# Kernel tuning notes

Measured on AMD Instinct MI355X. Metric: run time of the kernel, lower is better.

## Reference

```python
import math
import jax, jax.numpy as jnp
import numpy as np

D_MODEL = 256
NUM_FEATURES = 512  # 2 * d_model (module default)
BATCH, SEQ = 4, 4096
EPS = 1e-6
INPUT_SCALE = 0.25  # keeps exp(xW/sqrt(d) - ||x||^2/2) numerically meaningful


def _make_projection(key):
    # Orthogonal random features: ceil(M/d)=2 QR blocks, then sqrt(|gauss|) row scaling.
    k1, k2, k3 = jax.random.split(key, 3)
    q1, _ = jnp.linalg.qr(jax.random.normal(k1, (D_MODEL, D_MODEL), jnp.float32))
    q2, _ = jnp.linalg.qr(jax.random.normal(k2, (D_MODEL, D_MODEL), jnp.float32))
    proj = jnp.concatenate([q1, q2], axis=1)[:, :NUM_FEATURES]  # (d, M)
    scaling = jnp.sqrt(jnp.abs(jax.random.normal(k3, (D_MODEL, 1), jnp.float32)))
    return proj * scaling


def setup_inputs() -> dict:
    key = jax.random.key(0)
    kq, kk, kv, kp = jax.random.split(key, 4)
    shape = (BATCH, SEQ, D_MODEL)
    return {
        "query": jax.random.normal(kq, shape, jnp.float32) * INPUT_SCALE,
        "key": jax.random.normal(kk, shape, jnp.float32) * INPUT_SCALE,
        "value": jax.random.normal(kv, shape, jnp.float32) * INPUT_SCALE,
        "projection": _make_projection(kp),  # (d_model, num_features) buffer
    }


def _phi(x, projection):
    # phi(x) = exp(xW/sqrt(d) - ||x||^2/2) / sqrt(M)
    d = x.shape[-1]
    m = projection.shape[-1]
    proj = jnp.matmul(x, projection) / math.sqrt(d)  # (B, L, M)
    sq = 0.5 * jnp.sum(x * x, axis=-1, keepdims=True)  # (B, L, 1)
    return jnp.exp(proj - sq) / math.sqrt(m)


def reference(query, key, value, projection):
    qp = _phi(query, projection)  # (B, L, M)
    kp = _phi(key, projection)    # (B, L, M)
    B, L, M = qp.shape
    D = value.shape[-1]

    # Causal linear attention: running KV-state scan, O(B*M*D) state
    # (same math as cumsum of k' (outer) v, without materializing (B,L,M,D)).
    def step(carry, inp):
        kv_state, k_state = carry  # (B,M,D), (B,M)
        q_t, k_t, v_t = inp        # (B,M), (B,M), (B,D)
        kv_state = kv_state + k_t[:, :, None] * v_t[:, None, :]
        k_state = k_state + k_t
        num = jnp.einsum('bm,bmd->bd', q_t, kv_state)
        den = jnp.einsum('bm,bm->b', q_t, k_state)[:, None] + EPS
        return (kv_state, k_state), num / den

    init = (jnp.zeros((B, M, D), qp.dtype), jnp.zeros((B, M), qp.dtype))
    xs = (jnp.swapaxes(qp, 0, 1), jnp.swapaxes(kp, 0, 1), jnp.swapaxes(value, 0, 1))
    _, out = jax.lax.scan(step, init, xs)  # (L, B, D)
    return jnp.swapaxes(out, 0, 1)  # (B, L, D)
```

## Files before the change

kernel.cpp:

```cpp
#include <hip/hip_runtime.h>

#define B_ 4
#define L_ 4096
#define D_ 256
#define M_ 512
#define C_ 256
#define NC_ 16
#define NG_ (B_*NC_)
#define EPS_ 1e-6f
#define RSQRT_D_ 0.0625f
#define RSQRT_M_ 0.044194173824159216f

typedef __attribute__((ext_vector_type(8))) short short8;
typedef __attribute__((ext_vector_type(4))) short short4v;
typedef __attribute__((ext_vector_type(4))) float floatx4;

__device__ __forceinline__ short f2b(float f) {
  union { float f; unsigned u; } c; c.f = f;
  unsigned r = c.u + 0x7fffu + ((c.u >> 16) & 1u);
  return (short)(r >> 16);
}
__device__ __forceinline__ float b2f(short s) {
  union { unsigned u; float f; } c; c.u = ((unsigned)(unsigned short)s) << 16;
  return c.f;
}

__device__ __forceinline__ void async_copy16(const short* g, short* l) {
  __builtin_amdgcn_global_load_lds(
      (const __attribute__((address_space(1))) void*)(g),
      (__attribute__((address_space(3))) void*)(l), 16, 0, 0);
}

#define OFF_SB   0u
#define OFF_WT   16777216u
#define OFF_QP   17039360u
#define OFF_KP   33816576u
#define OFF_KPT  50593792u
#define OFF_VT   67371008u
#define OFF_AM   75759616u
#define OFF_PB   84148224u
#define OFF_ZP   100925440u

__device__ __forceinline__ void mfma_tile_gemm(
    const short* __restrict__ Ag, int lda,
    const short* __restrict__ Bg, int ldb,
    int K, short* sA, short* sB, floatx4 acc[4][4])
{
  const int tid  = threadIdx.x;
  const int lane = tid & 63;
  const int wave = tid >> 6;
  const int wm = wave >> 1, wn = wave & 1;
  const int q = lane >> 4, ml = lane & 15;

  for (int k0 = 0; k0 < K; k0 += 64) {
    #pragma unroll
    for (int it = 0; it < 4; ++it) {
      int s = tid + 256 * it;
      int m = s >> 3, k8 = s & 7;
      async_copy16(Ag + (size_t)m * lda + k0 + k8 * 8, sA + s * 8);
      async_copy16(Bg + (size_t)m * ldb + k0 + k8 * 8, sB + s * 8);
    }
    __syncthreads();
    #pragma unroll
    for (int ks = 0; ks < 2; ++ks) {
      short8 a[4], b[4];
      int k8 = ks * 4 + q;
      #pragma unroll
      for (int i = 0; i < 4; ++i) {
        int ra = wm * 64 + i * 16 + ml;
        a[i] = *(const short8*)(sA + (ra * 8 + k8) * 8);
        int rb = wn * 64 + i * 16 + ml;
        b[i] = *(const short8*)(sB + (rb * 8 + k8) * 8);
      }
      #pragma unroll
      for (int i = 0; i < 4; ++i)
        #pragma unroll
        for (int j = 0; j < 4; ++j)
          acc[i][j] = __builtin_amdgcn_mfma_f32_16x16x32_bf16(a[i], b[j], acc[i][j], 0, 0, 0);
    }
    __syncthreads();
  }
}

__global__ __launch_bounds__(256) void transpose_cvt_kernel(
    const float* __restrict__ v, const float* __restrict__ W,
    short* __restrict__ vT, short* __restrict__ Wt)
{
  const int z = blockIdx.z;
  const float* src; short* dst; int ld_in, ld_out;
  if (z < NG_) {
    if (blockIdx.x >= 4) return;
    src = v + (size_t)z * (C_*D_) + (size_t)blockIdx.y * 64 * D_ + blockIdx.x * 64;
    dst = vT + (size_t)z * (D_*C_) + (size_t)blockIdx.x * 64 * C_ + blockIdx.y * 64;
    ld_in = D_; ld_out = C_;
  } else {
    src = W + (size_t)blockIdx.y * 64 * M_ + blockIdx.x * 64;
    dst = Wt + (size_t)blockIdx.x * 64 * D_ + blockIdx.y * 64;
    ld_in = M_; ld_out = D_;
  }
  __shared__ short sm[64 * 65];
  const int tid = threadIdx.x;
  #pragma unroll
  for (int it = 0; it < 4; ++it) {
    int ci = tid + 256 * it;
    int row = ci >> 4, c4 = ci & 15;
    float4 x = *(const float4*)(src + (size_t)row * ld_in + c4 * 4);
    sm[(c4 * 4 + 0) * 65 + row] = f2b(x.x);
    sm[(c4 * 4 + 1) * 65 + row] = f2b(x.y);
    sm[(c4 * 4 + 2) * 65 + row] = f2b(x.z);
    sm[(c4 * 4 + 3) * 65 + row] = f2b(x.w);
  }
  __syncthreads();
  #pragma unroll
  for (int it = 0; it < 2; ++it) {
    int ci = tid + 256 * it;
    int dr = ci >> 3, t8 = ci & 7;
    short8 o;
    #pragma unroll
    for (int u = 0; u < 8; ++u) o[u] = sm[dr * 65 + t8 * 8 + u];
    *(short8*)(dst + (size_t)dr * ld_out + t8 * 8) = o;
  }
}

__global__ __launch_bounds__(512) void phi_mfma_kernel(
    const float* __restrict__ qin, const float* __restrict__ kin,
    const short* __restrict__ Wt,
    short* __restrict__ qp, short* __restrict__ kp, short* __restrict__ kpT,
    float* __restrict__ ZP)
{
  const bool is_k = (blockIdx.z == 1);
  const float* X = is_k ? kin : qin;
  short* outP = is_k ? kp : qp;
  const int idl = blockIdx.x + 2 * blockIdx.y;
  const int row0 = ((idl & 7) + 8 * (idl >> 4)) * 128;
  const int col0 = ((idl >> 3) & 1) * 256;
  __shared__ short smem[34816];
  __shared__ float zsb[512];
  __shared__ float sqs[128];
  short* sA = smem;
  short* sB = smem + 8192;
  const int tid = threadIdx.x, lane = tid & 63, wave = tid >> 6;
  const int wm = wave >> 2, wn = wave & 3, q = lane >> 4, ml = lane & 15;
  const int c8 = tid & 7, r8 = tid >> 3;
  floatx4 acc[4][4];
  #pragma unroll
  for (int i = 0; i < 4; ++i)
    #pragma unroll
    for (int j = 0; j < 4; ++j) acc[i][j] = (floatx4){0.f,0.f,0.f,0.f};

  float4 px0[2], px1[2];
  #pragma unroll
  for (int it = 0; it < 2; ++it) {
    const float* src = X + (size_t)(row0 + r8 + 64 * it) * D_ + c8 * 8;
    px0[it] = *(const float4*)src;
    px1[it] = *(const float4*)(src + 4);
  }
  short8 pw[4];
  #pragma unroll
  for (int it = 0; it < 4; ++it) {
    int mm = r8 + 64 * it;
    pw[it] = *(const short8*)(Wt + (size_t)(col0 + mm) * D_ + c8 * 8);
  }
  float ssq[2] = {0.f, 0.f};
  for (int k0 = 0; k0 < D_; k0 += 64) {
    #pragma unroll
    for (int it = 0; it < 2; ++it) {
      int m = r8 + 64 * it;
      float4 x0 = px0[it], x1 = px1[it];
      short8 vv;
      vv[0] = f2b(x0.x); vv[1] = f2b(x0.y); vv[2] = f2b(x0.z); vv[3] = f2b(x0.w);
      vv[4] = f2b(x1.x); vv[5] = f2b(x1.y); vv[6] = f2b(x1.z); vv[7] = f2b(x1.w);
      ssq[it] += x0.x*x0.x + x0.y*x0.y + x0.z*x0.z + x0.w*x0.w
               + x1.x*x1.x + x1.y*x1.y + x1.z*x1.z + x1.w*x1.w;
      *(short8*)(sA + (c8 * 128 + (m ^ c8)) * 8) = vv;
    }
    #pragma unroll
    for (int it = 0; it < 4; ++it) {
      int mm = r8 + 64 * it;
      *(short8*)(sB + (c8 * 256 + (mm ^ c8)) * 8) = pw[it];
    }
    if (k0 + 64 < D_) {
      #pragma unroll
      for (int it = 0; it < 2; ++it) {
        const float* src = X + (size_t)(row0 + r8 + 64 * it) * D_ + k0 + 64 + c8 * 8;
        px0[it] = *(const float4*)src;
        px1[it] = *(const float4*)(src + 4);
      }
      #pragma unroll
      for (int it = 0; it < 4; ++it) {
        int mm = r8 + 64 * it;
        pw[it] = *(const short8*)(Wt + (size_t)(col0 + mm) * D_ + k0 + 64 + c8 * 8);
      }
    }
    __syncthreads();
    #pragma unroll
    for (int ks = 0; ks < 2; ++ks) {
      short8 a[4], b[4];
      int kk = ks * 4 + q;
      #pragma unroll
      for (int i = 0; i < 4; ++i) {
        int ra = (wm * 64 + i * 16 + ml) ^ kk;
        a[i] = *(const short8*)(sA + (kk * 128 + ra) * 8);
        int rb = (wn * 64 + i * 16 + ml) ^ kk;
        b[i] = *(const short8*)(sB + (kk * 256 + rb) * 8);
      }
      #pragma unroll
      for (int i = 0; i < 4; ++i)
        #pragma unroll
        for (int j = 0; j < 4; ++j)
          acc[i][j] = __builtin_amdgcn_mfma_f32_16x16x32_bf16(a[i], b[j], acc[i][j], 0, 0, 0);
    }
    __syncthreads();
  }
  #pragma unroll
  for (int o = 1; o < 8; o <<= 1)
    #pragma unroll
    for (int it = 0; it < 2; ++it) ssq[it] += __shfl_xor(ssq[it], o);
  if (c8 == 0) {
    sqs[r8] = 0.5f * ssq[0];
    sqs[r8 + 64] = 0.5f * ssq[1];
  }
  __syncthreads();

  if (!is_k) {
    #pragma unroll
    for (int i = 0; i < 4; ++i) {
      int rl = wm * 64 + i * 16 + q * 4;
      float sqv[4];
      #pragma unroll
      for (int r = 0; r < 4; ++r) sqv[r] = sqs[rl + r];
      #pragma unroll
      for (int j = 0; j < 4; ++j) {
        int cl = wn * 64 + j * 16 + ml;
        #pragma unroll
        for (int r = 0; r < 4; ++r) {
          float pv = __expf(fmaf(acc[i][j][r], RSQRT_D_, -sqv[r])) * RSQRT_M_;
          smem[(size_t)(rl + r) * 264 + cl] = f2b(pv);
        }
      }
    }
    __syncthreads();
    #pragma unroll
    for (int it = 0; it < 8; ++it) {
      int idx = tid + 512 * it;
      int row = idx >> 5, cc8 = idx & 31;
      short8 vv = *(const short8*)(smem + (size_t)row * 264 + cc8 * 8);
      *(short8*)(outP + (size_t)(row0 + row) * M_ + col0 + cc8 * 8) = vv;
    }
  } else {
    float csum[4] = {0.f, 0.f, 0.f, 0.f};
    #pragma unroll
    for (int i = 0; i < 4; ++i) {
      int rl = wm * 64 + i * 16 + q * 4;
      float sqv[4];
      #pragma unroll
      for (int r = 0; r < 4; ++r) sqv[r] = sqs[rl + r];
      #pragma unroll
      for (int j = 0; j < 4; ++j) {
        int cl = wn * 64 + j * 16 + ml;
        short4v tb;
        #pragma unroll
        for (int r = 0; r < 4; ++r) {
          float pv = __expf(fmaf(acc[i][j][r], RSQRT_D_, -sqv[r])) * RSQRT_M_;
          short bv = f2b(pv);
          outP[(size_t)(row0 + rl + r) * M_ + col0 + cl] = bv;
          tb[r] = bv;
          csum[j] += b2f(bv);
        }
        *(short4v*)(smem + (size_t)cl * 136 + rl) = tb;
      }
    }
    #pragma unroll
    for (int j = 0; j < 4; ++j) {
      csum[j] += __shfl_xor(csum[j], 16);
      csum[j] += __shfl_xor(csum[j], 32);
    }
    if (lane < 16) {
      #pragma unroll
      for (int j = 0; j < 4; ++j)
        zsb[wm * 256 + wn * 64 + j * 16 + ml] = csum[j];
    }
    __syncthreads();
    int g = row0 >> 8, tb0 = row0 & 255;
    #pragma unroll
    for (int it = 0; it < 8; ++it) {
      int ci = tid + 512 * it;
      int t8 = ci & 15, cc = ci >> 4;
      short8 vv = *(const short8*)(smem + (size_t)cc * 136 + t8 * 8);
      *(short8*)(kpT + (size_t)g * (M_*C_) + (size_t)(col0 + cc) * C_ + tb0 + t8 * 8) = vv;
    }
    if (tid < 256) {
      float s = zsb[tid] + zsb[256 + tid];
      int p = (row0 >> 7) & 1;
      ZP[((size_t)g * 2 + p) * M_ + col0 + tid] = s;
    }
  }
}

__global__ __launch_bounds__(256) void mega_kernel(
    const short* __restrict__ vT, const short* __restrict__ kpT,
    const short* __restrict__ qp, const short* __restrict__ kp,
    short* __restrict__ Sb, short* __restrict__ Am)
{
  const int id = blockIdx.x + 4 * blockIdx.y + 12 * blockIdx.z;
  const int t12 = id >> 3;
  const int g  = (id & 7) + 8 * (t12 / 12);
  const int inner = t12 % 12;
  const int bx = inner & 3, by = inner >> 2;
  __shared__ short smem[17408];
  const int tid = threadIdx.x;

  floatx4 acc[4][4];
  #pragma unroll
  for (int i = 0; i < 4; ++i)
    #pragma unroll
    for (int j = 0; j < 4; ++j) acc[i][j] = (floatx4){0.f,0.f,0.f,0.f};
  const int lane = tid & 63, wave = tid >> 6;
  const int wm = wave >> 1, wn = wave & 1, q = lane >> 4, ln = lane & 15;

  if (by < 2) {
    const int m0 = bx * 128, d0 = by * 128;
    mfma_tile_gemm(vT + (size_t)g * (D_*C_) + (size_t)d0 * C_, C_,
                   kpT + (size_t)g * (M_*C_) + (size_t)m0 * C_, C_, C_,
                   smem, smem + 8192, acc);
    #pragma unroll
    for (int i = 0; i < 4; ++i) {
      int lr = wm * 64 + i * 16 + q * 4;
      #pragma unroll
      for (int j = 0; j < 4; ++j) {
        int lc = wn * 64 + j * 16 + ln;
        #pragma unroll
        for (int r = 0; r < 4; ++r)
          smem[(size_t)(lr + r) * 136 + lc] = f2b(acc[i][j][r]);
      }
    }
    __syncthreads();
    #pragma unroll
    for (int it = 0; it < 8; ++it) {
      int idx = tid + 256 * it;
      int row = idx >> 4, c8 = idx & 15;
      short8 vv = *(const short8*)(smem + (size_t)row * 136 + c8 * 8);
      *(short8*)(Sb + ((size_t)g * D_ + d0 + row) * M_ + m0 + c8 * 8) = vv;
    }
  } else {
    const int tt0 = (bx >> 1) * 128, tp0 = (bx & 1) * 128;
    short* Ag = Am + (size_t)g * (C_*C_);
    if (tp0 > tt0) {
      short8 z8 = 0;
      #pragma unroll
      for (int it = 0; it < 8; ++it) {
        int ci = tid + 256 * it;
        int row = ci >> 4, c8 = ci & 15;
        *(short8*)(Ag + (size_t)(tt0 + row) * C_ + tp0 + c8 * 8) = z8;
      }
      return;
    }
    const size_t cb = (size_t)g * C_;
    mfma_tile_gemm(qp + (cb + tt0) * M_, M_, kp + (cb + tp0) * M_, M_, M_,
                   smem, smem + 8192, acc);
    #pragma unroll
    for (int i = 0; i < 4; ++i) {
      int lr = wm * 64 + i * 16 + q * 4;
      #pragma unroll
      for (int j = 0; j < 4; ++j) {
        int lc = wn * 64 + j * 16 + ln;
        #pragma unroll
        for (int r = 0; r < 4; ++r) {
          short bv = ((tp0 + lc) <= (tt0 + lr + r)) ? f2b(acc[i][j][r]) : (short)0;
          smem[(size_t)(lr + r) * 136 + lc] = bv;
        }
      }
    }
    __syncthreads();
    #pragma unroll
    for (int it = 0; it < 8; ++it) {
      int idx = tid + 256 * it;
      int row = idx >> 4, c8 = idx & 15;
      short8 vv = *(const short8*)(smem + (size_t)row * 136 + c8 * 8);
      *(short8*)(Ag + (size_t)(tt0 + row) * C_ + tp0 + c8 * 8) = vv;
    }
  }
}

__global__ __launch_bounds__(256) void prefixS_kernel(
    const short* __restrict__ Sb, short* __restrict__ Pb,
    const float* __restrict__ ZP, float* __restrict__ ZPX)
{
  if (blockIdx.x >= 256) {
    int idx = (blockIdx.x - 256) * 256 + threadIdx.x;
    int b = idx >> 9, m = idx & 511;
    float run = 0.f;
    #pragma unroll
    for (int i = 0; i < NC_; ++i) {
      int g = b * NC_ + i;
      ZPX[(size_t)g * M_ + m] = run;
      run += ZP[((size_t)g * 2 + 0) * M_ + m] + ZP[((size_t)g * 2 + 1) * M_ + m];
    }
    return;
  }
  int j = blockIdx.x * 256 + threadIdx.x;
  int b = j >> 14, e8 = j & 16383;
  size_t base = ((size_t)b * NC_) * 131072 + (size_t)e8 * 8;
  short8 t[NC_];
  #pragma unroll
  for (int i = 0; i < NC_; ++i)
    t[i] = *(const short8*)(Sb + base + (size_t)i * 131072);
  float run[8] = {0.f,0.f,0.f,0.f,0.f,0.f,0.f,0.f};
  #pragma unroll
  for (int i = 0; i < NC_; ++i) {
    short8 o;
    #pragma unroll
    for (int u = 0; u < 8; ++u) { o[u] = f2b(run[u]); run[u] += b2f(t[i][u]); }
    *(short8*)(Pb + base + (size_t)i * 131072) = o;
  }
}

__global__ __launch_bounds__(256) void out_mfma_kernel(
    const short* __restrict__ qp, const short* __restrict__ Pb,
    const short* __restrict__ Am, const short* __restrict__ vT,
    const float* __restrict__ ZPX, float* __restrict__ out)
{
  const int id = blockIdx.x + 2 * blockIdx.y + 8 * blockIdx.z;
  const int g  = (id & 7) + 8 * (id >> 6);
  const int inner = (id >> 3) & 7;
  const int d0 = (inner & 1) * 128, tt0 = (inner >> 1) * 64;
  __shared__ short smem[16896];
  __shared__ float zbuf[512];
  __shared__ float dbuf[64];
  short* sA = smem; short* sB = smem + 4096;
  const int tid = threadIdx.x, lane = tid & 63, wave = tid >> 6;
  const int wm = wave >> 1, wn = wave & 1, q = lane >> 4, ml = lane & 15;
  const int r8 = tid >> 3;

  {
    zbuf[tid]       = ZPX[(size_t)g * M_ + tid];
    zbuf[tid + 256] = ZPX[(size_t)g * M_ + 256 + tid];
    if (tid < 64) dbuf[tid] = 0.f;
  }
  __syncthreads();

  floatx4 acc[2][4];
  #pragma unroll
  for (int i = 0; i < 2; ++i)
    #pragma unroll
    for (int j = 0; j < 4; ++j) acc[i][j] = (floatx4){0.f,0.f,0.f,0.f};

  {
    const short* Ag = qp + ((size_t)g * C_ + tt0) * M_;
    const short* Bg = Pb + (size_t)g * (D_*M_) + (size_t)d0 * M_;
    float dp[2] = {0.f, 0.f};
    short8 pa[2], pb[4];
    #pragma unroll
    for (int it = 0; it < 2; ++it) {
      int ci = tid + 256 * it;
      int m = ci >> 3, k8 = ci & 7;
      pa[it] = *(const short8*)(Ag + (size_t)m * M_ + k8 * 8);
    }
    #pragma unroll
    for (int it = 0; it < 4; ++it) {
      int ci = tid + 256 * it;
      int m = ci >> 3, k8 = ci & 7;
      pb[it] = *(const short8*)(Bg + (size_t)m * M_ + k8 * 8);
    }
    for (int k0 = 0; k0 < M_; k0 += 64) {
      #pragma unroll
      for (int it = 0; it < 2; ++it) {
        int ci = tid + 256 * it;
        int m = ci >> 3, k8 = ci & 7;
        int dst = (k8 >> 2) * 256 + (m >> 4) * 64 + (k8 & 3) * 16 + ((m & 15) ^ k8);
        *(short8*)(sA + dst * 8) = pa[it];
        const float* zz = zbuf + k0 + k8 * 8;
        float d = 0.f;
        #pragma unroll
        for (int u = 0; u < 8; ++u) d = fmaf(b2f(pa[it][u]), zz[u], d);
        dp[it] += d;
      }
      #pragma unroll
      for (int it = 0; it < 4; ++it) {
        int ci = tid + 256 * it;
        int m = ci >> 3, k8 = ci & 7;
        int dst = (k8 >> 2) * 512 + (m >> 4) * 64 + (k8 & 3) * 16 + ((m & 15) ^ k8);
        *(short8*)(sB + dst * 8) = pb[it];
      }
      if (k0 + 64 < M_) {
        #pragma unroll
        for (int it = 0; it < 2; ++it) {
          int ci = tid + 256 * it;
          int m = ci >> 3, k8 = ci & 7;
          pa[it] = *(const short8*)(Ag + (size_t)m * M_ + k0 + 64 + k8 * 8);
        }
        #pragma unroll
        for (int it = 0; it < 4; ++it) {
          int ci = tid + 256 * it;
          int m = ci >> 3, k8 = ci & 7;
          pb[it] = *(const short8*)(Bg + (size_t)m * M_ + k0 + 64 + k8 * 8);
        }
      }
      __syncthreads();
      #pragma unroll
      for (int ks = 0; ks < 2; ++ks) {
        short8 a[2], b[4];
        int k8 = ks * 4 + q;
        #pragma unroll
        for (int i = 0; i < 2; ++i) {
          int ca = ks * 256 + (wm * 2 + i) * 64 + q * 16 + (ml ^ k8);
          a[i] = *(const short8*)(sA + ca * 8);
        }
        #pragma unroll
        for (int j = 0; j < 4; ++j) {
          int cb = ks * 512 + (wn * 4 + j) * 64 + q * 16 + (ml ^ k8);
          b[j] = *(const short8*)(sB + cb * 8);
        }
        #pragma unroll
        for (int i = 0; i < 2; ++i)
          #pragma unroll
          for (int j = 0; j < 4; ++j)
            acc[i][j] = __builtin_amdgcn_mfma_f32_16x16x32_bf16(a[i], b[j], acc[i][j], 0, 0, 0);
      }
      __syncthreads();
    }
    #pragma unroll
    for (int o = 1; o < 8; o <<= 1)
      #pragma unroll
      for (int it = 0; it < 2; ++it) dp[it] += __shfl_xor(dp[it], o);
    if ((tid & 7) == 0) {
      #pragma unroll
      for (int it = 0; it < 2; ++it) dbuf[r8 + 32 * it] += dp[it];
    }
  }

  {
    const short* Ag = Am + ((size_t)g * C_ + tt0) * C_;
    const short* Bg = vT + (size_t)g * (D_*C_) + (size_t)d0 * C_;
    float dp[2] = {0.f, 0.f};
    short8 pa[2], pb[4];
    #pragma unroll
    for (int it = 0; it < 2; ++it) {
      int ci = tid + 256 * it;
      int m = ci >> 3, k8 = ci & 7;
      pa[it] = *(const short8*)(Ag + (size_t)m * C_ + k8 * 8);
    }
    #pragma unroll
    for (int it = 0; it < 4; ++it) {
      int ci = tid + 256 * it;
      int m = ci >> 3, k8 = ci & 7;
      pb[it] = *(const short8*)(Bg + (size_t)m * C_ + k8 * 8);
    }
    for (int k0 = 0; k0 < C_; k0 += 64) {
      #pragma unroll
      for (int it = 0; it < 2; ++it) {
        int ci = tid + 256 * it;
        int m = ci >> 3, k8 = ci & 7;
        int dst = (k8 >> 2) * 256 + (m >> 4) * 64 + (k8 & 3) * 16 + ((m & 15) ^ k8);
        *(short8*)(sA + dst * 8) = pa[it];
        float d = 0.f;
        #pragma unroll
        for (int u = 0; u < 8; ++u) d += b2f(pa[it][u]);
        dp[it] += d;
      }
      #pragma unroll
      for (int it = 0; it < 4; ++it) {
        int ci = tid + 256 * it;
        int m = ci >> 3, k8 = ci & 7;
        int dst = (k8 >> 2) * 512 + (m >> 4) * 64 + (k8 & 3) * 16 + ((m & 15) ^ k8);
        *(short8*)(sB + dst * 8) = pb[it];
      }
      if (k0 + 64 < C_) {
        #pragma unroll
        for (int it = 0; it < 2; ++it) {
          int ci = tid + 256 * it;
          int m = ci >> 3, k8 = ci & 7;
          pa[it] = *(const short8*)(Ag + (size_t)m * C_ + k0 + 64 + k8 * 8);
        }
        #pragma unroll
        for (int it = 0; it < 4; ++it) {
          int ci = tid + 256 * it;
          int m = ci >> 3, k8 = ci & 7;
          pb[it] = *(const short8*)(Bg + (size_t)m * C_ + k0 + 64 + k8 * 8);
        }
      }
      __syncthreads();
      #pragma unroll
      for (int ks = 0; ks < 2; ++ks) {
        short8 a[2], b[4];
        int k8 = ks * 4 + q;
        #pragma unroll
        for (int i = 0; i < 2; ++i) {
          int ca = ks * 256 + (wm * 2 + i) * 64 + q * 16 + (ml ^ k8);
          a[i] = *(const short8*)(sA + ca * 8);
        }
        #pragma unroll
        for (int j = 0; j < 4; ++j) {
          int cb = ks * 512 + (wn * 4 + j) * 64 + q * 16 + (ml ^ k8);
          b[j] = *(const short8*)(sB + cb * 8);
        }
        #pragma unroll
        for (int i = 0; i < 2; ++i)
          #pragma unroll
          for (int j = 0; j < 4; ++j)
            acc[i][j] = __builtin_amdgcn_mfma_f32_16x16x32_bf16(a[i], b[j], acc[i][j], 0, 0, 0);
      }
      __syncthreads();
    }
    #pragma unroll
    for (int o = 1; o < 8; o <<= 1)
      #pragma unroll
      for (int it = 0; it < 2; ++it) dp[it] += __shfl_xor(dp[it], o);
    if ((tid & 7) == 0) {
      #pragma unroll
      for (int it = 0; it < 2; ++it) dbuf[r8 + 32 * it] += dp[it];
    }
  }
  __syncthreads();

  float* smF = (float*)smem;
  #pragma unroll
  for (int i = 0; i < 2; ++i) {
    int lr = wm * 32 + i * 16 + q * 4;
    #pragma unroll
    for (int r = 0; r < 4; ++r) {
      float rc = 1.0f / (dbuf[lr + r] + EPS_);
      #pragma unroll
      for (int j = 0; j < 4; ++j) {
        int lc = wn * 64 + j * 16 + ml;
        smF[(size_t)(lr + r) * 132 + lc] = acc[i][j][r] * rc;
      }
    }
  }
  __syncthreads();
  #pragma unroll
  for (int it = 0; it < 8; ++it) {
    int idx = tid + 256 * it;
    int row = idx >> 5, c4 = idx & 31;
    float4 val = *(const float4*)(smF + (size_t)row * 132 + c4 * 4);
    *(float4*)(out + (size_t)(g * C_ + tt0 + row) * D_ + d0 + c4 * 4) = val;
  }
}

extern "C" void kernel_launch(void* const* d_in, const int* in_sizes, int n_in,
                              void* d_out, int out_size, void* d_ws, size_t ws_size,
                              hipStream_t stream) {
  const float* q = (const float*)d_in[0];
  const float* k = (const float*)d_in[1];
  const float* v = (const float*)d_in[2];
  const float* W = (const float*)d_in[3];
  float* out = (float*)d_out;
  char* ws = (char*)d_ws;

  short* Sb  = (short*)(ws + OFF_SB);
  short* Wt  = (short*)(ws + OFF_WT);
  short* qp  = (short*)(ws + OFF_QP);
  short* kp  = (short*)(ws + OFF_KP);
  short* kpT = (short*)(ws + OFF_KPT);
  short* vT  = (short*)(ws + OFF_VT);
  short* Am  = (short*)(ws + OFF_AM);
  short* Pb  = (short*)(ws + OFF_PB);
  float* ZP  = (float*)(ws + OFF_ZP);
  float* ZPX = (float*)(ws + OFF_WT);

  transpose_cvt_kernel<<<dim3(8, 4, NG_ + 1), 256, 0, stream>>>(v, W, vT, Wt);
  phi_mfma_kernel<<<dim3(2, 128, 2), 512, 0, stream>>>(q, k, Wt, qp, kp, kpT, ZP);
  mega_kernel<<<dim3(4, 3, NG_), 256, 0, stream>>>(vT, kpT, qp, kp, Sb, Am);
  prefixS_kernel<<<264, 256, 0, stream>>>(Sb, Pb, ZP, ZPX);
  out_mfma_kernel<<<dim3(2, 4, NG_), 256, 0, stream>>>(qp, Pb, Am, vT, ZPX, out);
}
```

Baseline: 159.3 us.

## Register-prefetch GEMM tiles with swizzled LDS and lighter barriers

The shared mfma_tile_gemm drops the global_load_lds async copies. It now prefetches the next K-tile into registers while the current tile sits in LDS, and stores it with an XOR-swizzled layout to cut LDS bank conflicts. Across all GEMM loops, __syncthreads is replaced by a custom barrier that waits only on lgkmcnt (LDS) before s_barrier, so outstanding global prefetch loads are not drained at each barrier. This raises register pressure, and correctness now depends on the compiler inserting vmcnt waits before the prefetched registers are used.

Result: no change. 157.3 us (-1.2%).

```diff
diff --git a/kernel.cpp b/kernel.cpp
--- a/kernel.cpp
+++ b/kernel.cpp
@@ -25,10 +25,8 @@
   return c.f;
 }
 
-__device__ __forceinline__ void async_copy16(const short* g, short* l) {
-  __builtin_amdgcn_global_load_lds(
-      (const __attribute__((address_space(1))) void*)(g),
-      (__attribute__((address_space(3))) void*)(l), 16, 0, 0);
+__device__ __forceinline__ void wg_barrier_lgkm() {
+  asm volatile("s_waitcnt lgkmcnt(0)\n\ts_barrier" ::: "memory");
 }
 
 #define OFF_SB   0u
@@ -52,25 +50,43 @@
   const int wm = wave >> 1, wn = wave & 1;
   const int q = lane >> 4, ml = lane & 15;
 
+  short8 pa[4], pb[4];
+  #pragma unroll
+  for (int it = 0; it < 4; ++it) {
+    int ci = tid + 256 * it;
+    int m = ci >> 3, k8 = ci & 7;
+    pa[it] = *(const short8*)(Ag + (size_t)m * lda + k8 * 8);
+    pb[it] = *(const short8*)(Bg + (size_t)m * ldb + k8 * 8);
+  }
   for (int k0 = 0; k0 < K; k0 += 64) {
     #pragma unroll
     for (int it = 0; it < 4; ++it) {
-      int s = tid + 256 * it;
-      int m = s >> 3, k8 = s & 7;
-      async_copy16(Ag + (size_t)m * lda + k0 + k8 * 8, sA + s * 8);
-      async_copy16(Bg + (size_t)m * ldb + k0 + k8 * 8, sB + s * 8);
-    }
-    __syncthreads();
+      int ci = tid + 256 * it;
+      int m = ci >> 3, k8 = ci & 7;
+      int dst = (k8 >> 2) * 512 + (m >> 4) * 64 + (k8 & 3) * 16 + ((m & 15) ^ k8);
+      *(short8*)(sA + dst * 8) = pa[it];
+      *(short8*)(sB + dst * 8) = pb[it];
+    }
+    if (k0 + 64 < K) {
+      #pragma unroll
+      for (int it = 0; it < 4; ++it) {
+        int ci = tid + 256 * it;
+        int m = ci >> 3, k8 = ci & 7;
+        pa[it] = *(const short8*)(Ag + (size_t)m * lda + k0 + 64 + k8 * 8);
+        pb[it] = *(const short8*)(Bg + (size_t)m * ldb + k0 + 64 + k8 * 8);
+      }
+    }
+    wg_barrier_lgkm();
     #pragma unroll
     for (int ks = 0; ks < 2; ++ks) {
       short8 a[4], b[4];
       int k8 = ks * 4 + q;
       #pragma unroll
       for (int i = 0; i < 4; ++i) {
-        int ra = wm * 64 + i * 16 + ml;
-        a[i] = *(const short8*)(sA + (ra * 8 + k8) * 8);
-        int rb = wn * 64 + i * 16 + ml;
-        b[i] = *(const short8*)(sB + (rb * 8 + k8) * 8);
+        int ca = ks * 512 + (wm * 4 + i) * 64 + q * 16 + (ml ^ k8);
+        a[i] = *(const short8*)(sA + ca * 8);
+        int cb = ks * 512 + (wn * 4 + i) * 64 + q * 16 + (ml ^ k8);
+        b[i] = *(const short8*)(sB + cb * 8);
       }
       #pragma unroll
       for (int i = 0; i < 4; ++i)
@@ -78,7 +94,7 @@
         for (int j = 0; j < 4; ++j)
           acc[i][j] = __builtin_amdgcn_mfma_f32_16x16x32_bf16(a[i], b[j], acc[i][j], 0, 0, 0);
     }
-    __syncthreads();
+    wg_barrier_lgkm();
   }
 }
 
@@ -192,7 +208,7 @@
         pw[it] = *(const short8*)(Wt + (size_t)(col0 + mm) * D_ + k0 + 64 + c8 * 8);
       }
     }
-    __syncthreads();
+    wg_barrier_lgkm();
     #pragma unroll
     for (int ks = 0; ks < 2; ++ks) {
       short8 a[4], b[4];
@@ -210,7 +226,7 @@
         for (int j = 0; j < 4; ++j)
           acc[i][j] = __builtin_amdgcn_mfma_f32_16x16x32_bf16(a[i], b[j], acc[i][j], 0, 0, 0);
     }
-    __syncthreads();
+    wg_barrier_lgkm();
   }
   #pragma unroll
   for (int o = 1; o < 8; o <<= 1)
@@ -496,7 +512,7 @@
           pb[it] = *(const short8*)(Bg + (size_t)m * M_ + k0 + 64 + k8 * 8);
         }
       }
-      __syncthreads();
+      wg_barrier_lgkm();
       #pragma unroll
       for (int ks = 0; ks < 2; ++ks) {
         short8 a[2], b[4];
@@ -517,7 +533,7 @@
           for (int j = 0; j < 4; ++j)
             acc[i][j] = __builtin_amdgcn_mfma_f32_16x16x32_bf16(a[i], b[j], acc[i][j], 0, 0, 0);
       }
-      __syncthreads();
+      wg_barrier_lgkm();
     }
     #pragma unroll
     for (int o = 1; o < 8; o <<= 1)
@@ -579,7 +595,7 @@
           pb[it] = *(const short8*)(Bg + (size_t)m * C_ + k0 + 64 + k8 * 8);
         }
       }
-      __syncthreads();
+      wg_barrier_lgkm();
       #pragma unroll
       for (int ks = 0; ks < 2; ++ks) {
         short8 a[2], b[4];
@@ -600,7 +616,7 @@
           for (int j = 0; j < 4; ++j)
             acc[i][j] = __builtin_amdgcn_mfma_f32_16x16x32_bf16(a[i], b[j], acc[i][j], 0, 0, 0);
       }
-      __syncthreads();
+      wg_barrier_lgkm();
     }
     #pragma unroll
     for (int o = 1; o < 8; o <<= 1)
```
